# Optimization experiments

Hardware: AMD Instinct MI355X
Metric: run time of the kernel (lower is better)

Reference implementation:

```python
import jax, jax.numpy as jnp
import numpy as np

MAX_DISP = 24  # 192 // (2**(3+1)/2**1)


def build_cost_volume(feat_l, feat_r, max_disp=MAX_DISP):
    # Faithful to the torch loop: cost[:, d, :, x] = sum_c |feat_l[..,x] - feat_r[..,x-d]|
    # with feat_r treated as zero for x < d (matches feat_l.abs().sum(1) branch).
    B, C, h, w = feat_l.shape
    pad = jnp.pad(feat_r, ((0, 0), (0, 0), (0, 0), (max_disp - 1, 0)))  # zero left-pad
    # idx[d, x] = x - d shifted into padded coords; x-d < 0 hits the zero pad.
    idx = (max_disp - 1) + jnp.arange(w)[None, :] - jnp.arange(max_disp)[:, None]  # [D, w]
    shifted = pad[:, :, :, idx]  # [B, C, h, D, w]
    cost = jnp.abs(feat_l[:, :, :, None, :] - shifted).sum(axis=1)  # [B, h, D, w]
    return jnp.transpose(cost, (0, 2, 1, 3))  # [B, D, h, w]


def bilinear_resize_align_corners(x, H, W):
    # F.interpolate(mode='bilinear', align_corners=True)
    B, C, h, w = x.shape
    ys = jnp.linspace(0.0, h - 1.0, H)
    xs = jnp.linspace(0.0, w - 1.0, W)
    y0 = jnp.floor(ys).astype(jnp.int32)
    y1 = jnp.minimum(y0 + 1, h - 1)
    wy = (ys - y0)[:, None]                 # [H, 1]
    x0 = jnp.floor(xs).astype(jnp.int32)
    x1 = jnp.minimum(x0 + 1, w - 1)
    wx = xs - x0                             # [W]
    rows = x[:, :, y0, :] * (1.0 - wy) + x[:, :, y1, :] * wy   # [B, C, H, w]
    out = rows[:, :, :, x0] * (1.0 - wx) + rows[:, :, :, x1] * wx  # [B, C, H, W]
    return out


def setup_inputs() -> dict:
    key = jax.random.key(0)
    k1, k2 = jax.random.split(key)
    B, C, h, w = 16, 4, 128, 240  # features at 1/8 of a 1024x1920 stereo pair
    feat_l = jax.random.normal(k1, (B, C, h, w), dtype=jnp.float32)
    feat_r = jax.random.normal(k2, (B, C, h, w), dtype=jnp.float32)
    return {"feat_l": feat_l, "feat_r": feat_r, "img_h": 1024, "img_w": 1920}


def reference(feat_l, feat_r, img_h, img_w):
    cost = build_cost_volume(feat_l, feat_r)            # [B, D, h, w]
    p = jax.nn.softmax(-cost, axis=1)                   # softmax over disparity bins
    disp = jnp.arange(MAX_DISP, dtype=feat_l.dtype).reshape(1, -1, 1, 1)
    pred = jnp.sum(p * disp, axis=1, keepdims=True)     # [B, 1, h, w]
    pred = pred * (float(img_h) / pred.shape[2])        # rescale disparity to full-res units
    return bilinear_resize_align_corners(pred, img_h, img_w)  # [B, 1, img_h, img_w]
```

## Files before the change

### kernel.cpp

```cpp
#include <hip/hip_runtime.h>
#include <math.h>

#define BB 16
#define CC 4
#define HH 128
#define WW 240
#define MAXD 24
#define OH 1024
#define OW 1920

__global__ __launch_bounds__(256) void pred_kernel(const float* __restrict__ fl,
                                                   const float* __restrict__ fr,
                                                   float* __restrict__ pred) {
    const int row = blockIdx.x;
    const int b = row / HH;
    const int y = row - b * HH;
    const int x = threadIdx.x;

    __shared__ float sL[CC][WW];
    __shared__ float sR[CC][WW + MAXD - 1];

    #pragma unroll
    for (int c = 0; c < CC; ++c) {
        const size_t idx = (((size_t)b * CC + c) * HH + y) * WW;
        if (x < WW) {
            sL[c][x] = fl[idx + x];
            sR[c][x + MAXD - 1] = fr[idx + x];
        }
        if (x < MAXD - 1) sR[c][x] = 0.0f;
    }
    __syncthreads();
    if (x >= WW) return;

    const float l0 = sL[0][x], l1 = sL[1][x], l2 = sL[2][x], l3 = sL[3][x];

    float cost[MAXD];
    float m = 1e30f;
    #pragma unroll
    for (int d = 0; d < MAXD; ++d) {
        const int xi = x - d + (MAXD - 1);
        const float cv = fabsf(l0 - sR[0][xi]) + fabsf(l1 - sR[1][xi])
                       + fabsf(l2 - sR[2][xi]) + fabsf(l3 - sR[3][xi]);
        cost[d] = cv;
        m = fminf(m, cv);
    }
    float s = 0.0f, wsum = 0.0f;
    #pragma unroll
    for (int d = 0; d < MAXD; ++d) {
        const float p = __expf(m - cost[d]);
        s += p;
        wsum += p * (float)d;
    }
    pred[(size_t)row * WW + x] = 8.0f * (wsum / s);
}

__global__ __launch_bounds__(256) void resize_kernel(const float* __restrict__ pred,
                                                     float* __restrict__ out) {
    const int tid = blockIdx.x * blockDim.x + threadIdx.x;
    const int QW = OW / 4;
    const int xq = tid % QW;
    const int rest = tid / QW;
    const int oy = rest % OH;
    const int b = rest / OH;

    const float sy = (float)(HH - 1) / (float)(OH - 1);
    const float sx = (float)(WW - 1) / (float)(OW - 1);

    const float ysf = (float)oy * sy;
    int y0 = (int)ysf;
    if (y0 > HH - 1) y0 = HH - 1;
    const int y1 = min(y0 + 1, HH - 1);
    const float wy = ysf - (float)y0;

    const float* __restrict__ row0 = pred + ((size_t)b * HH + y0) * WW;
    const float* __restrict__ row1 = pred + ((size_t)b * HH + y1) * WW;

    float4 o;
    float* op = &o.x;
    #pragma unroll
    for (int i = 0; i < 4; ++i) {
        const int ox = xq * 4 + i;
        const float xsf = (float)ox * sx;
        int x0 = (int)xsf;
        if (x0 > WW - 1) x0 = WW - 1;
        const int x1 = min(x0 + 1, WW - 1);
        const float wx = xsf - (float)x0;
        const float r0 = row0[x0] + (row0[x1] - row0[x0]) * wx;
        const float r1 = row1[x0] + (row1[x1] - row1[x0]) * wx;
        op[i] = r0 + (r1 - r0) * wy;
    }
    ((float4*)out)[tid] = o;
}

extern "C" void kernel_launch(void* const* d_in, const int* in_sizes, int n_in,
                              void* d_out, int out_size, void* d_ws, size_t ws_size,
                              hipStream_t stream) {
    const float* feat_l = (const float*)d_in[0];
    const float* feat_r = (const float*)d_in[1];
    float* out = (float*)d_out;
    float* pred = (float*)d_ws;

    pred_kernel<<<BB * HH, 256, 0, stream>>>(feat_l, feat_r, pred);

    const int total_q = BB * OH * (OW / 4);
    resize_kernel<<<total_q / 256, 256, 0, stream>>>(pred, out);
}
```

Measured before the change: 151.3 us.

## Fuse cost-volume softmax and bilinear upsample into one kernel per source row

Replaces the two-kernel pipeline with a single kernel where each block owns one low-res row pair (y0, y0+1). It computes the disparity prediction for both rows in shared memory and interpolates them horizontally into a shared buffer. It then writes every output row whose floor source row is y0 with float4 stores. This drops the intermediate pred round trip through global memory and one kernel launch, at the cost of computing each low-res row twice and a short serial loop over output rows per block.

```diff
diff --git a/kernel.cpp b/kernel.cpp
--- a/kernel.cpp
+++ b/kernel.cpp
@@ -9,87 +9,104 @@
 #define OH 1024
 #define OW 1920
 
-__global__ __launch_bounds__(256) void pred_kernel(const float* __restrict__ fl,
-                                                   const float* __restrict__ fr,
-                                                   float* __restrict__ pred) {
-    const int row = blockIdx.x;
-    const int b = row / HH;
-    const int y = row - b * HH;
-    const int x = threadIdx.x;
+__global__ __launch_bounds__(256) void fused_kernel(const float* __restrict__ fl,
+                                                    const float* __restrict__ fr,
+                                                    float* __restrict__ out) {
+    const int blk = blockIdx.x;
+    const int b = blk >> 7;
+    const int y0 = blk & (HH - 1);
+    const int y1 = min(y0 + 1, HH - 1);
+    const int tid = threadIdx.x;
 
-    __shared__ float sL[CC][WW];
-    __shared__ float sR[CC][WW + MAXD - 1];
+    __shared__ float sR[2][CC][WW + MAXD - 1];
+    __shared__ float sP[2][WW];
+    __shared__ float vx[2][OW];
 
-    #pragma unroll
-    for (int c = 0; c < CC; ++c) {
-        const size_t idx = (((size_t)b * CC + c) * HH + y) * WW;
-        if (x < WW) {
-            sL[c][x] = fl[idx + x];
-            sR[c][x + MAXD - 1] = fr[idx + x];
-        }
-        if (x < MAXD - 1) sR[c][x] = 0.0f;
+    const int rows2[2] = {y0, y1};
+
+    for (int i = tid; i < 2 * CC * WW; i += 256) {
+        const int r = i / (CC * WW);
+        const int rem = i - r * (CC * WW);
+        const int c = rem / WW;
+        const int x = rem - c * WW;
+        sR[r][c][x + MAXD - 1] = fr[(((size_t)b * CC + c) * HH + rows2[r]) * WW + x];
+    }
+    for (int i = tid; i < 2 * CC * (MAXD - 1); i += 256) {
+        const int r = i / (CC * (MAXD - 1));
+        const int rem = i - r * (CC * (MAXD - 1));
+        const int c = rem / (MAXD - 1);
+        const int x = rem - c * (MAXD - 1);
+        sR[r][c][x] = 0.0f;
     }
     __syncthreads();
-    if (x >= WW) return;
 
-    const float l0 = sL[0][x], l1 = sL[1][x], l2 = sL[2][x], l3 = sL[3][x];
+    for (int j = tid; j < 2 * WW; j += 256) {
+        const int r = j / WW;
+        const int x = j - r * WW;
+        const size_t g = (((size_t)b * CC) * HH + rows2[r]) * WW + x;
+        const float l0 = fl[g];
+        const float l1 = fl[g + (size_t)HH * WW];
+        const float l2 = fl[g + 2 * (size_t)HH * WW];
+        const float l3 = fl[g + 3 * (size_t)HH * WW];
+        float cost[MAXD];
+        float m = 1e30f;
+#pragma unroll
+        for (int d = 0; d < MAXD; ++d) {
+            const int xi = x - d + MAXD - 1;
+            const float cv = fabsf(l0 - sR[r][0][xi]) + fabsf(l1 - sR[r][1][xi])
+                           + fabsf(l2 - sR[r][2][xi]) + fabsf(l3 - sR[r][3][xi]);
+            cost[d] = cv;
+            m = fminf(m, cv);
+        }
+        float s = 0.0f, wsum = 0.0f;
+#pragma unroll
+        for (int d = 0; d < MAXD; ++d) {
+            const float p = __expf(m - cost[d]);
+            s += p;
+            wsum += p * (float)d;
+        }
+        sP[r][x] = 8.0f * (wsum / s);
+    }
+    __syncthreads();
 
-    float cost[MAXD];
-    float m = 1e30f;
-    #pragma unroll
-    for (int d = 0; d < MAXD; ++d) {
-        const int xi = x - d + (MAXD - 1);
-        const float cv = fabsf(l0 - sR[0][xi]) + fabsf(l1 - sR[1][xi])
-                       + fabsf(l2 - sR[2][xi]) + fabsf(l3 - sR[3][xi]);
-        cost[d] = cv;
-        m = fminf(m, cv);
-    }
-    float s = 0.0f, wsum = 0.0f;
-    #pragma unroll
-    for (int d = 0; d < MAXD; ++d) {
-        const float p = __expf(m - cost[d]);
-        s += p;
-        wsum += p * (float)d;
-    }
-    pred[(size_t)row * WW + x] = 8.0f * (wsum / s);
-}
-
-__global__ __launch_bounds__(256) void resize_kernel(const float* __restrict__ pred,
-                                                     float* __restrict__ out) {
-    const int tid = blockIdx.x * blockDim.x + threadIdx.x;
-    const int QW = OW / 4;
-    const int xq = tid % QW;
-    const int rest = tid / QW;
-    const int oy = rest % OH;
-    const int b = rest / OH;
-
-    const float sy = (float)(HH - 1) / (float)(OH - 1);
-    const float sx = (float)(WW - 1) / (float)(OW - 1);
-
-    const float ysf = (float)oy * sy;
-    int y0 = (int)ysf;
-    if (y0 > HH - 1) y0 = HH - 1;
-    const int y1 = min(y0 + 1, HH - 1);
-    const float wy = ysf - (float)y0;
-
-    const float* __restrict__ row0 = pred + ((size_t)b * HH + y0) * WW;
-    const float* __restrict__ row1 = pred + ((size_t)b * HH + y1) * WW;
-
-    float4 o;
-    float* op = &o.x;
-    #pragma unroll
-    for (int i = 0; i < 4; ++i) {
-        const int ox = xq * 4 + i;
-        const float xsf = (float)ox * sx;
+    const float sxf = (float)(WW - 1) / (float)(OW - 1);
+    for (int i = tid; i < 2 * OW; i += 256) {
+        const int r = i / OW;
+        const int ox = i - r * OW;
+        const float xsf = (float)ox * sxf;
         int x0 = (int)xsf;
         if (x0 > WW - 1) x0 = WW - 1;
         const int x1 = min(x0 + 1, WW - 1);
         const float wx = xsf - (float)x0;
-        const float r0 = row0[x0] + (row0[x1] - row0[x0]) * wx;
-        const float r1 = row1[x0] + (row1[x1] - row1[x0]) * wx;
-        op[i] = r0 + (r1 - r0) * wy;
+        const float a = sP[r][x0];
+        vx[r][ox] = a + (sP[r][x1] - a) * wx;
     }
-    ((float4*)out)[tid] = o;
+    __syncthreads();
+
+    const float syf = (float)(HH - 1) / (float)(OH - 1);
+    const int base = (int)((float)y0 * ((float)(OH - 1) / (float)(HH - 1))) - 2;
+    const float4* __restrict__ v0p = (const float4*)vx[0];
+    const float4* __restrict__ v1p = (const float4*)vx[1];
+    for (int k = 0; k < 13; ++k) {
+        const int oy = base + k;
+        if (oy < 0 || oy >= OH) continue;
+        const float ysf = (float)oy * syf;
+        int yy = (int)ysf;
+        if (yy > HH - 1) yy = HH - 1;
+        if (yy != y0) continue;
+        const float wy = ysf - (float)yy;
+        float4* __restrict__ orow = (float4*)(out + ((size_t)b * OH + oy) * OW);
+        for (int q = tid; q < OW / 4; q += 256) {
+            const float4 v0 = v0p[q];
+            const float4 v1 = v1p[q];
+            float4 o;
+            o.x = v0.x + (v1.x - v0.x) * wy;
+            o.y = v0.y + (v1.y - v0.y) * wy;
+            o.z = v0.z + (v1.z - v0.z) * wy;
+            o.w = v0.w + (v1.w - v0.w) * wy;
+            orow[q] = o;
+        }
+    }
 }
 
 extern "C" void kernel_launch(void* const* d_in, const int* in_sizes, int n_in,
@@ -98,10 +115,5 @@
     const float* feat_l = (const float*)d_in[0];
     const float* feat_r = (const float*)d_in[1];
     float* out = (float*)d_out;
-    float* pred = (float*)d_ws;
-
-    pred_kernel<<<BB * HH, 256, 0, stream>>>(feat_l, feat_r, pred);
-
-    const int total_q = BB * OH * (OW / 4);
-    resize_kernel<<<total_q / 256, 256, 0, stream>>>(pred, out);
+    fused_kernel<<<BB * HH, 256, 0, stream>>>(feat_l, feat_r, out);
 }
```

Result: no change. 153.3 us (+1.3%).
